# Performance work log

Hardware: AMD Instinct MI355X
Metric: run time of the kernel (lower is better)

The kernel has to match this reference:

```python
import jax, jax.numpy as jnp
import numpy as np

B, FR, T, C = 8, 257, 300, 64
CPP, G, K = 16, 8, 3
EPS = 1e-5


def _ln(x, g, b):
    m = jnp.mean(x, axis=-1, keepdims=True)
    v = jnp.mean((x - m) ** 2, axis=-1, keepdims=True)
    return (x - m) * jax.lax.rsqrt(v + EPS) * g + b


def _freq_conv(x, g, b, w, cb, alpha):
    # x: [N, F, C]
    res = x
    y = _ln(x, g, b).transpose(0, 2, 1)  # [N, C, F]
    y = jax.lax.conv_general_dilated(
        y, w, window_strides=(1,), padding=((K // 2, K // 2),),
        feature_group_count=G, dimension_numbers=("NCH", "OIH", "NCH"))
    y = y + cb[None, :, None]
    y = y.transpose(0, 2, 1)  # [N, F, C]
    return res + jnp.where(y >= 0, y, alpha * y)


def _full_band(x, g, b, rw, rb, fW, fB, ew, eb):
    # x: [N, F, C]
    res = x
    y = _ln(x, g, b)
    hp = jax.nn.silu(jnp.einsum("nfc,pc->nfp", y, rw) + rb)  # [N, F, Cpp]
    hp = hp.transpose(0, 2, 1)  # [N, Cpp, F]
    # batched per-channel Linear(F, F): out[n,c,g] = sum_f hp[n,c,f] * fW[c,g,f] + fB[c,g]
    hp = jnp.einsum("ncf,cgf->ncg", hp, fW) + fB[None]
    hp = hp.transpose(0, 2, 1)  # [N, F, Cpp]
    out = jax.nn.silu(jnp.einsum("nfp,cp->nfc", hp, ew) + eb)
    return res + out


def setup_inputs() -> dict:
    key = jax.random.key(0)
    ks = jax.random.split(key, 20)
    s = 0.05
    d = {
        "h": jax.random.normal(ks[0], (B, FR, T, C), jnp.float32),
        "fc1_g": jnp.ones((C,), jnp.float32),
        "fc1_b": jnp.zeros((C,), jnp.float32),
        "fc1_w": jax.random.normal(ks[1], (C, C // G, K), jnp.float32) * s,
        "fc1_cb": jax.random.normal(ks[2], (C,), jnp.float32) * s,
        "fc1_a": jnp.asarray(0.25, jnp.float32),
        "fbl_g": jnp.ones((C,), jnp.float32),
        "fbl_b": jnp.zeros((C,), jnp.float32),
        "red_w": jax.random.normal(ks[3], (CPP, C), jnp.float32) * s,
        "red_b": jax.random.normal(ks[4], (CPP,), jnp.float32) * s,
        "fW": jax.random.normal(ks[5], (CPP, FR, FR), jnp.float32) * s,
        "fB": jax.random.normal(ks[6], (CPP, FR), jnp.float32) * s,
        "exp_w": jax.random.normal(ks[7], (C, CPP), jnp.float32) * s,
        "exp_b": jax.random.normal(ks[8], (C,), jnp.float32) * s,
        "fc2_g": jnp.ones((C,), jnp.float32),
        "fc2_b": jnp.zeros((C,), jnp.float32),
        "fc2_w": jax.random.normal(ks[9], (C, C // G, K), jnp.float32) * s,
        "fc2_cb": jax.random.normal(ks[10], (C,), jnp.float32) * s,
        "fc2_a": jnp.asarray(0.25, jnp.float32),
    }
    return d


def reference(h, fc1_g, fc1_b, fc1_w, fc1_cb, fc1_a,
              fbl_g, fbl_b, red_w, red_b, fW, fB, exp_w, exp_b,
              fc2_g, fc2_b, fc2_w, fc2_cb, fc2_a):
    b, fr, t, c = h.shape
    x = h.transpose(0, 2, 1, 3).reshape(b * t, fr, c)  # [B*T, F, C]
    x = _freq_conv(x, fc1_g, fc1_b, fc1_w, fc1_cb, fc1_a)
    x = _full_band(x, fbl_g, fbl_b, red_w, red_b, fW, fB, exp_w, exp_b)
    x = _freq_conv(x, fc2_g, fc2_b, fc2_w, fc2_cb, fc2_a)
    return x.reshape(b, t, fr, c).transpose(0, 2, 1, 3)
```

## Files before the change

kernel.cpp:

```cpp
#include <hip/hip_runtime.h>
#include <math.h>

#define BDIM 8
#define FR   257
#define TT   300
#define CC   64
#define NN   (BDIM*TT)
#define CPPC 16
#define GG   8
#define CPG  8
#define KW   3
#define EPSV 1e-5f

#define FT    36
#define NTIL  8
#define ROWS  38
#define FSTR  65
#define NIT   10

#define X1_ELEMS ((size_t)NN*FR*CC)
#define HP_ELEMS ((size_t)CPPC*NN*FR)

template<int CTRL>
__device__ __forceinline__ float dpp_term(float v) {
    return __int_as_float(
        __builtin_amdgcn_update_dpp(0, __float_as_int(v), CTRL, 0xf, 0xf, true));
}
template<int PAT>
__device__ __forceinline__ float swz_term(float v) {
    return __int_as_float(__builtin_amdgcn_ds_swizzle(__float_as_int(v), PAT));
}

__device__ __forceinline__ float wave_sum64(float v) {
    v += dpp_term<0x111>(v);
    v += dpp_term<0x112>(v);
    v += dpp_term<0x114>(v);
    v += dpp_term<0x118>(v);
    v += dpp_term<0x142>(v);
    v += dpp_term<0x143>(v);
    return __int_as_float(__builtin_amdgcn_readlane(__float_as_int(v), 63));
}

__device__ __forceinline__ void ln_stats_dpp(float v, float& m, float& r) {
    float s  = wave_sum64(v);
    float ss = wave_sum64(v*v);
    m = s * (1.0f/64.0f);
    float var = ss * (1.0f/64.0f) - m*m;
    r = rsqrtf(var + EPSV);
}

__device__ __forceinline__ float conv_row(float y0, float y1, float y2,
                                          const float wq[8][KW]) {
    float q[8];
    #pragma unroll
    for (int d = 0; d < 8; ++d)
        q[d] = y0*wq[d][0] + y1*wq[d][1] + y2*wq[d][2];
    float acc = q[0];
    acc += dpp_term<0xB1>(q[1]);
    acc += dpp_term<0x4E>(q[2]);
    acc += dpp_term<0x1B>(q[3]);
    acc += swz_term<0x101F>(q[4]);
    acc += swz_term<0x141F>(q[5]);
    acc += swz_term<0x181F>(q[6]);
    acc += dpp_term<0x141>(q[7]);
    return acc;
}

__global__ __launch_bounds__(256, 8)
void k_fc1(const float* __restrict__ h,
           const float* __restrict__ g1, const float* __restrict__ b1,
           const float* __restrict__ w1, const float* __restrict__ cb1,
           const float* __restrict__ a1,
           const float* __restrict__ g2, const float* __restrict__ b2,
           const float* __restrict__ redw, const float* __restrict__ redb,
           float* __restrict__ x1, float* __restrict__ hpT)
{
    __shared__ float ys[ROWS*FSTR];
    __shared__ float xs[FT*FSTR];

    const int n  = blockIdx.x;
    const int f0 = blockIdx.y * FT;
    const int nf = min(FT, FR - f0);
    const int b = n / TT, t = n - b*TT;
    const int tid = threadIdx.x;
    const int lane = tid & 63, wid = tid >> 6;

    const float alpha = a1[0];
    const float gA = g1[lane], bA = b1[lane];
    const float gB = g2[lane], bB = b2[lane];
    const float cbv = cb1[lane];

    const size_t hb0 = ((size_t)b*FR*TT + t)*CC;
    #pragma unroll
    for (int it = 0; it < NIT; ++it) {
        int lr = wid + it*4;
        if (lr >= ROWS) continue;
        int f = f0 - 1 + lr;
        if (f >= 0 && f < FR) {
            float v = h[hb0 + (size_t)f*TT*CC + lane];
            if (lr >= 1 && lr <= nf) xs[(lr-1)*FSTR + lane] = v;
            float m, r; ln_stats_dpp(v, m, r);
            ys[lr*FSTR + lane] = (v - m) * r * gA + bA;
        } else {
            ys[lr*FSTR + lane] = 0.0f;
        }
    }
    __syncthreads();

    const int l8 = lane & 7;
    const int gbase = lane & 56;
    float wq[8][KW];
    #pragma unroll
    for (int d = 0; d < 8; ++d) {
        const float* wp = w1 + (size_t)(gbase | (l8 ^ d))*(CPG*KW) + l8*KW;
        #pragma unroll
        for (int k = 0; k < KW; ++k) wq[d][k] = wp[k];
    }

    #pragma unroll
    for (int it = 0; it < NIT; ++it) {
        int lr = wid + it*4;
        if (lr < 1 || lr > nf) continue;
        float y0 = ys[(lr-1)*FSTR + lane];
        float y1 = ys[ lr   *FSTR + lane];
        float y2 = ys[(lr+1)*FSTR + lane];
        float acc = conv_row(y0, y1, y2, wq) + cbv;
        float pr = acc >= 0.0f ? acc : alpha*acc;
        float xv = xs[(lr-1)*FSTR + lane] + pr;
        xs[(lr-1)*FSTR + lane] = xv;
        int f = f0 + lr - 1;
        x1[(size_t)n*FR*CC + (size_t)f*CC + lane] = xv;
    }
    __syncthreads();

    #pragma unroll
    for (int it = 0; it < NIT; ++it) {
        int lr = wid + it*4;
        if (lr < 1 || lr > nf) continue;
        float v = xs[(lr-1)*FSTR + lane];
        float m, r; ln_stats_dpp(v, m, r);
        ys[lr*FSTR + lane] = (v - m) * r * gB + bB;
    }
    __syncthreads();

    {
        const int L = lane;
        const int lr = (L < nf) ? (L + 1) : 1;
        const int p0 = wid * 4;
        const float* wp0 = redw + (size_t)(p0+0)*CC;
        const float* wp1 = redw + (size_t)(p0+1)*CC;
        const float* wp2 = redw + (size_t)(p0+2)*CC;
        const float* wp3 = redw + (size_t)(p0+3)*CC;
        float a0 = redb[p0+0], a1v = redb[p0+1], a2 = redb[p0+2], a3 = redb[p0+3];
        #pragma unroll 16
        for (int c = 0; c < CC; ++c) {
            float yv = ys[lr*FSTR + c];
            a0  += yv * wp0[c];
            a1v += yv * wp1[c];
            a2  += yv * wp2[c];
            a3  += yv * wp3[c];
        }
        if (L < nf) {
            int f = f0 + L;
            float s0 = a0  / (1.0f + expf(-a0));
            float s1 = a1v / (1.0f + expf(-a1v));
            float s2 = a2  / (1.0f + expf(-a2));
            float s3 = a3  / (1.0f + expf(-a3));
            size_t base = (size_t)n*FR + f;
            hpT[(size_t)(p0+0)*(NN*FR) + base] = s0;
            hpT[(size_t)(p0+1)*(NN*FR) + base] = s1;
            hpT[(size_t)(p0+2)*(NN*FR) + base] = s2;
            hpT[(size_t)(p0+3)*(NN*FR) + base] = s3;
        }
    }
}

#define GBM 128
#define GBN 64
#define GBK 16
#define GLDA 132
#define GLDB 68

__global__ __launch_bounds__(128, 2)
void k_fgemm(const float* __restrict__ hpT, const float* __restrict__ fW,
             const float* __restrict__ fB, float* __restrict__ hp2T)
{
    __shared__ __align__(16) float As[GBK*GLDA];
    __shared__ __align__(16) float Bs[GBK*GLDB];
    const int c  = blockIdx.z;
    const int m0 = blockIdx.x * GBM;
    const int f0 = blockIdx.y * GBN;
    const int tid = threadIdx.x;
    const int tx = tid & 7;
    const int ty = tid >> 3;

    const float* Ab = hpT + (size_t)c*(NN*FR);
    const float* Bb = fW  + (size_t)c*(FR*FR);

    float acc[8][8];
    #pragma unroll
    for (int i = 0; i < 8; ++i)
        #pragma unroll
        for (int j = 0; j < 8; ++j) acc[i][j] = 0.0f;

    for (int k0 = 0; k0 < FR; k0 += GBK) {
        #pragma unroll
        for (int l = 0; l < 4; ++l) {
            int e = tid + l*128;
            int m = e >> 2, kq = e & 3;
            int gm = m0 + m, gk = k0 + kq*4;
            float4 v = make_float4(0.f,0.f,0.f,0.f);
            if (gm < NN) {
                if (gk + 3 < FR) {
                    v = *reinterpret_cast<const float4*>(&Ab[(size_t)gm*FR + gk]);
                } else {
                    float tv[4] = {0.f,0.f,0.f,0.f};
                    #pragma unroll
                    for (int j = 0; j < 4; ++j) if (gk+j < FR) tv[j] = Ab[(size_t)gm*FR + gk + j];
                    v = make_float4(tv[0],tv[1],tv[2],tv[3]);
                }
            }
            As[(kq*4+0)*GLDA + m] = v.x;
            As[(kq*4+1)*GLDA + m] = v.y;
            As[(kq*4+2)*GLDA + m] = v.z;
            As[(kq*4+3)*GLDA + m] = v.w;
        }
        #pragma unroll
        for (int l = 0; l < 2; ++l) {
            int e = tid + l*128;
            int j = e >> 2, kq = e & 3;
            int gf = f0 + j, gk = k0 + kq*4;
            float4 v = make_float4(0.f,0.f,0.f,0.f);
            if (gf < FR) {
                if (gk + 3 < FR) {
                    v = *reinterpret_cast<const float4*>(&Bb[(size_t)gf*FR + gk]);
                } else {
                    float tv[4] = {0.f,0.f,0.f,0.f};
                    #pragma unroll
                    for (int jj = 0; jj < 4; ++jj) if (gk+jj < FR) tv[jj] = Bb[(size_t)gf*FR + gk + jj];
                    v = make_float4(tv[0],tv[1],tv[2],tv[3]);
                }
            }
            Bs[(kq*4+0)*GLDB + j] = v.x;
            Bs[(kq*4+1)*GLDB + j] = v.y;
            Bs[(kq*4+2)*GLDB + j] = v.z;
            Bs[(kq*4+3)*GLDB + j] = v.w;
        }
        __syncthreads();

        #pragma unroll
        for (int k = 0; k < GBK; ++k) {
            const float4 a0 = *reinterpret_cast<const float4*>(&As[k*GLDA + ty*8]);
            const float4 a1 = *reinterpret_cast<const float4*>(&As[k*GLDA + ty*8 + 4]);
            const float4 b0 = *reinterpret_cast<const float4*>(&Bs[k*GLDB + tx*8]);
            const float4 b1 = *reinterpret_cast<const float4*>(&Bs[k*GLDB + tx*8 + 4]);
            const float av[8] = {a0.x,a0.y,a0.z,a0.w,a1.x,a1.y,a1.z,a1.w};
            const float bv[8] = {b0.x,b0.y,b0.z,b0.w,b1.x,b1.y,b1.z,b1.w};
            #pragma unroll
            for (int i = 0; i < 8; ++i)
                #pragma unroll
                for (int j = 0; j < 8; ++j)
                    acc[i][j] += av[i]*bv[j];
        }
        __syncthreads();
    }

    #pragma unroll
    for (int i = 0; i < 8; ++i) {
        int m = m0 + ty*8 + i;
        if (m >= NN) continue;
        #pragma unroll
        for (int j = 0; j < 8; ++j) {
            int fr = f0 + tx*8 + j;
            if (fr < FR)
                hp2T[(size_t)c*(NN*FR) + (size_t)m*FR + fr] = acc[i][j] + fB[c*FR + fr];
        }
    }
}

__global__ __launch_bounds__(256, 8)
void k_fc2(const float* __restrict__ x1, const float* __restrict__ hp2T,
           const float* __restrict__ expw, const float* __restrict__ expb,
           const float* __restrict__ g3, const float* __restrict__ b3,
           const float* __restrict__ w2, const float* __restrict__ cb2,
           const float* __restrict__ a2,
           float* __restrict__ out)
{
    __shared__ float ys[ROWS*FSTR];
    __shared__ float xs[FT*FSTR];

    const int n  = blockIdx.x;
    const int f0 = blockIdx.y * FT;
    const int nf = min(FT, FR - f0);
    const int b = n / TT, t = n - b*TT;
    const int tid = threadIdx.x;
    const int lane = tid & 63, wid = tid >> 6;

    const float ebv = expb[lane];
    const float gC = g3[lane], bC = b3[lane];
    const float alpha = a2[0];
    const float cbv = cb2[lane];

    float ew[CPPC];
    #pragma unroll
    for (int p = 0; p < CPPC; ++p) ew[p] = expw[lane*CPPC + p];

    #pragma unroll
    for (int it = 0; it < NIT; ++it) {
        int lr = wid + it*4;
        if (lr >= ROWS) continue;
        int f = f0 - 1 + lr;
        if (f >= 0 && f < FR) {
            size_t base = (size_t)n*FR + f;
            float z = ebv;
            #pragma unroll
            for (int p = 0; p < CPPC; ++p)
                z += hp2T[(size_t)p*(NN*FR) + base] * ew[p];
            float sg = z / (1.0f + expf(-z));
            float v = x1[(size_t)n*FR*CC + (size_t)f*CC + lane] + sg;
            if (lr >= 1 && lr <= nf) xs[(lr-1)*FSTR + lane] = v;
            float m, r; ln_stats_dpp(v, m, r);
            ys[lr*FSTR + lane] = (v - m) * r * gC + bC;
        } else {
            ys[lr*FSTR + lane] = 0.0f;
        }
    }
    __syncthreads();

    const int l8 = lane & 7;
    const int gbase = lane & 56;
    float wq[8][KW];
    #pragma unroll
    for (int d = 0; d < 8; ++d) {
        const float* wp = w2 + (size_t)(gbase | (l8 ^ d))*(CPG*KW) + l8*KW;
        #pragma unroll
        for (int k = 0; k < KW; ++k) wq[d][k] = wp[k];
    }

    const size_t ob0 = ((size_t)b*FR*TT + t)*CC;
    #pragma unroll
    for (int it = 0; it < NIT; ++it) {
        int lr = wid + it*4;
        if (lr < 1 || lr > nf) continue;
        float y0 = ys[(lr-1)*FSTR + lane];
        float y1 = ys[ lr   *FSTR + lane];
        float y2 = ys[(lr+1)*FSTR + lane];
        float acc = conv_row(y0, y1, y2, wq) + cbv;
        float pr = acc >= 0.0f ? acc : alpha*acc;
        int f = f0 + lr - 1;
        out[ob0 + (size_t)f*TT*CC + lane] = xs[(lr-1)*FSTR + lane] + pr;
    }
}

extern "C" void kernel_launch(void* const* d_in, const int* in_sizes, int n_in,
                              void* d_out, int out_size, void* d_ws, size_t ws_size,
                              hipStream_t stream) {
    const float* h      = (const float*)d_in[0];
    const float* fc1_g  = (const float*)d_in[1];
    const float* fc1_b  = (const float*)d_in[2];
    const float* fc1_w  = (const float*)d_in[3];
    const float* fc1_cb = (const float*)d_in[4];
    const float* fc1_a  = (const float*)d_in[5];
    const float* fbl_g  = (const float*)d_in[6];
    const float* fbl_b  = (const float*)d_in[7];
    const float* red_w  = (const float*)d_in[8];
    const float* red_b  = (const float*)d_in[9];
    const float* fW     = (const float*)d_in[10];
    const float* fB     = (const float*)d_in[11];
    const float* exp_w  = (const float*)d_in[12];
    const float* exp_b  = (const float*)d_in[13];
    const float* fc2_g  = (const float*)d_in[14];
    const float* fc2_b  = (const float*)d_in[15];
    const float* fc2_w  = (const float*)d_in[16];
    const float* fc2_cb = (const float*)d_in[17];
    const float* fc2_a  = (const float*)d_in[18];

    float* ws   = (float*)d_ws;
    float* x1   = ws;
    float* hpT  = x1 + X1_ELEMS;
    float* hp2T = hpT + HP_ELEMS;

    dim3 g1(NN, NTIL);
    k_fc1<<<g1, 256, 0, stream>>>(h, fc1_g, fc1_b, fc1_w, fc1_cb, fc1_a,
                                  fbl_g, fbl_b, red_w, red_b, x1, hpT);

    dim3 g2((NN + GBM - 1)/GBM, (FR + GBN - 1)/GBN, CPPC);
    k_fgemm<<<g2, 128, 0, stream>>>(hpT, fW, fB, hp2T);

    dim3 g3(NN, NTIL);
    k_fc2<<<g3, 256, 0, stream>>>(x1, hp2T, exp_w, exp_b,
                                  fc2_g, fc2_b, fc2_w, fc2_cb, fc2_a,
                                  (float*)d_out);
}
```

Baseline: 990.4 us.

## Enlarge frequency tiles and process two rows per wave with float2 LayerNorm

Grows the per-block frequency tile in the two conv kernels from 36 to 64 rows, which shrinks the fraction of halo rows that are reloaded and normalised twice. Each wave now handles two rows at once, one per 32-lane half, using float2 global loads and a half-wave DPP/swizzle reduction for the LayerNorm statistics. The load and normalisation loops are restructured to match, and launch bounds are relaxed from 8 to 2 blocks per CU. In exchange each block needs more LDS and the register budget grows, which may lower occupancy, and the tail tile at the end of the frequency axis is partly empty.

```diff
diff --git a/kernel.cpp b/kernel.cpp
--- a/kernel.cpp
+++ b/kernel.cpp
@@ -12,11 +12,10 @@
 #define KW   3
 #define EPSV 1e-5f
 
-#define FT    36
-#define NTIL  8
-#define ROWS  38
+#define FT    64
+#define NTIL  5
+#define ROWS  66
 #define FSTR  65
-#define NIT   10
 
 #define X1_ELEMS ((size_t)NN*FR*CC)
 #define HP_ELEMS ((size_t)CPPC*NN*FR)
@@ -31,19 +30,16 @@
     return __int_as_float(__builtin_amdgcn_ds_swizzle(__float_as_int(v), PAT));
 }
 
-__device__ __forceinline__ float wave_sum64(float v) {
-    v += dpp_term<0x111>(v);
-    v += dpp_term<0x112>(v);
-    v += dpp_term<0x114>(v);
-    v += dpp_term<0x118>(v);
-    v += dpp_term<0x142>(v);
-    v += dpp_term<0x143>(v);
-    return __int_as_float(__builtin_amdgcn_readlane(__float_as_int(v), 63));
-}
-
-__device__ __forceinline__ void ln_stats_dpp(float v, float& m, float& r) {
-    float s  = wave_sum64(v);
-    float ss = wave_sum64(v*v);
+__device__ __forceinline__ void ln_stats_pair(float2 v, float& m, float& r) {
+    float s  = v.x + v.y;
+    float ss = v.x*v.x + v.y*v.y;
+    s += dpp_term<0x111>(s);  ss += dpp_term<0x111>(ss);
+    s += dpp_term<0x112>(s);  ss += dpp_term<0x112>(ss);
+    s += dpp_term<0x114>(s);  ss += dpp_term<0x114>(ss);
+    s += dpp_term<0x118>(s);  ss += dpp_term<0x118>(ss);
+    s += dpp_term<0x142>(s);  ss += dpp_term<0x142>(ss);
+    s  = swz_term<0x03E0>(s);
+    ss = swz_term<0x03E0>(ss);
     m = s * (1.0f/64.0f);
     float var = ss * (1.0f/64.0f) - m*m;
     r = rsqrtf(var + EPSV);
@@ -66,7 +62,14 @@
     return acc;
 }
 
-__global__ __launch_bounds__(256, 8)
+__device__ __forceinline__ void lds_wr2(float* p, int idx, float2 v) {
+    p[idx] = v.x; p[idx+1] = v.y;
+}
+__device__ __forceinline__ float2 lds_rd2(const float* p, int idx) {
+    return make_float2(p[idx], p[idx+1]);
+}
+
+__global__ __launch_bounds__(256, 2)
 void k_fc1(const float* __restrict__ h,
            const float* __restrict__ g1, const float* __restrict__ b1,
            const float* __restrict__ w1, const float* __restrict__ cb1,
@@ -84,25 +87,28 @@
     const int b = n / TT, t = n - b*TT;
     const int tid = threadIdx.x;
     const int lane = tid & 63, wid = tid >> 6;
-
-    const float alpha = a1[0];
-    const float gA = g1[lane], bA = b1[lane];
-    const float gB = g2[lane], bB = b2[lane];
-    const float cbv = cb1[lane];
+    const int hl = lane & 31, half = lane >> 5;
+    const int ch = hl << 1;
+
+    const float2 gA2 = *reinterpret_cast<const float2*>(&g1[ch]);
+    const float2 bA2 = *reinterpret_cast<const float2*>(&b1[ch]);
 
     const size_t hb0 = ((size_t)b*FR*TT + t)*CC;
     #pragma unroll
-    for (int it = 0; it < NIT; ++it) {
-        int lr = wid + it*4;
-        if (lr >= ROWS) continue;
+    for (int it = 0; it < 9; ++it) {
+        int rp = wid + it*4;
+        if (rp >= 33) continue;
+        int lr = 2*rp + half;
         int f = f0 - 1 + lr;
         if (f >= 0 && f < FR) {
-            float v = h[hb0 + (size_t)f*TT*CC + lane];
-            if (lr >= 1 && lr <= nf) xs[(lr-1)*FSTR + lane] = v;
-            float m, r; ln_stats_dpp(v, m, r);
-            ys[lr*FSTR + lane] = (v - m) * r * gA + bA;
+            float2 v = *reinterpret_cast<const float2*>(&h[hb0 + (size_t)f*TT*CC + ch]);
+            if (lr >= 1 && lr <= nf) lds_wr2(xs, (lr-1)*FSTR + ch, v);
+            float m, r; ln_stats_pair(v, m, r);
+            float2 o = make_float2((v.x - m)*r*gA2.x + bA2.x,
+                                   (v.y - m)*r*gA2.y + bA2.y);
+            lds_wr2(ys, lr*FSTR + ch, o);
         } else {
-            ys[lr*FSTR + lane] = 0.0f;
+            lds_wr2(ys, lr*FSTR + ch, make_float2(0.f, 0.f));
         }
     }
     __syncthreads();
@@ -116,9 +122,11 @@
         #pragma unroll
         for (int k = 0; k < KW; ++k) wq[d][k] = wp[k];
     }
-
-    #pragma unroll
-    for (int it = 0; it < NIT; ++it) {
+    const float alpha = a1[0];
+    const float cbv = cb1[lane];
+
+    #pragma unroll
+    for (int it = 0; it < 17; ++it) {
         int lr = wid + it*4;
         if (lr < 1 || lr > nf) continue;
         float y0 = ys[(lr-1)*FSTR + lane];
@@ -133,13 +141,18 @@
     }
     __syncthreads();
 
-    #pragma unroll
-    for (int it = 0; it < NIT; ++it) {
-        int lr = wid + it*4;
-        if (lr < 1 || lr > nf) continue;
-        float v = xs[(lr-1)*FSTR + lane];
-        float m, r; ln_stats_dpp(v, m, r);
-        ys[lr*FSTR + lane] = (v - m) * r * gB + bB;
+    const float2 gB2 = *reinterpret_cast<const float2*>(&g2[ch]);
+    const float2 bB2 = *reinterpret_cast<const float2*>(&b2[ch]);
+    #pragma unroll
+    for (int it = 0; it < 8; ++it) {
+        int rp = wid + it*4;
+        int ir = 2*rp + half;
+        if (ir >= nf) continue;
+        float2 v = lds_rd2(xs, ir*FSTR + ch);
+        float m, r; ln_stats_pair(v, m, r);
+        float2 o = make_float2((v.x - m)*r*gB2.x + bB2.x,
+                               (v.y - m)*r*gB2.y + bB2.y);
+        lds_wr2(ys, (ir+1)*FSTR + ch, o);
     }
     __syncthreads();
 
@@ -278,7 +291,7 @@
     }
 }
 
-__global__ __launch_bounds__(256, 8)
+__global__ __launch_bounds__(256, 2)
 void k_fc2(const float* __restrict__ x1, const float* __restrict__ hp2T,
            const float* __restrict__ expw, const float* __restrict__ expb,
            const float* __restrict__ g3, const float* __restrict__ b3,
@@ -295,34 +308,44 @@
     const int b = n / TT, t = n - b*TT;
     const int tid = threadIdx.x;
     const int lane = tid & 63, wid = tid >> 6;
-
-    const float ebv = expb[lane];
-    const float gC = g3[lane], bC = b3[lane];
-    const float alpha = a2[0];
-    const float cbv = cb2[lane];
-
-    float ew[CPPC];
-    #pragma unroll
-    for (int p = 0; p < CPPC; ++p) ew[p] = expw[lane*CPPC + p];
-
-    #pragma unroll
-    for (int it = 0; it < NIT; ++it) {
-        int lr = wid + it*4;
-        if (lr >= ROWS) continue;
+    const int hl = lane & 31, half = lane >> 5;
+    const int ch = hl << 1;
+
+    const float2 gC2 = *reinterpret_cast<const float2*>(&g3[ch]);
+    const float2 bC2 = *reinterpret_cast<const float2*>(&b3[ch]);
+    const float2 eb2 = *reinterpret_cast<const float2*>(&expb[ch]);
+
+    float2 ew2[CPPC];
+    #pragma unroll
+    for (int p = 0; p < CPPC; ++p)
+        ew2[p] = make_float2(expw[ch*CPPC + p], expw[(ch+1)*CPPC + p]);
+
+    #pragma unroll
+    for (int it = 0; it < 9; ++it) {
+        int rp = wid + it*4;
+        if (rp >= 33) continue;
+        int lr = 2*rp + half;
         int f = f0 - 1 + lr;
         if (f >= 0 && f < FR) {
             size_t base = (size_t)n*FR + f;
-            float z = ebv;
+            float2 z = eb2;
             #pragma unroll
-            for (int p = 0; p < CPPC; ++p)
-                z += hp2T[(size_t)p*(NN*FR) + base] * ew[p];
-            float sg = z / (1.0f + expf(-z));
-            float v = x1[(size_t)n*FR*CC + (size_t)f*CC + lane] + sg;
-            if (lr >= 1 && lr <= nf) xs[(lr-1)*FSTR + lane] = v;
-            float m, r; ln_stats_dpp(v, m, r);
-            ys[lr*FSTR + lane] = (v - m) * r * gC + bC;
+            for (int p = 0; p < CPPC; ++p) {
+                float hp = hp2T[(size_t)p*(NN*FR) + base];
+                z.x += hp * ew2[p].x;
+                z.y += hp * ew2[p].y;
+            }
+            float2 sg = make_float2(z.x / (1.0f + expf(-z.x)),
+                                    z.y / (1.0f + expf(-z.y)));
+            float2 xv = *reinterpret_cast<const float2*>(&x1[(size_t)n*FR*CC + (size_t)f*CC + ch]);
+            float2 v = make_float2(xv.x + sg.x, xv.y + sg.y);
+            if (lr >= 1 && lr <= nf) lds_wr2(xs, (lr-1)*FSTR + ch, v);
+            float m, r; ln_stats_pair(v, m, r);
+            float2 o = make_float2((v.x - m)*r*gC2.x + bC2.x,
+                                   (v.y - m)*r*gC2.y + bC2.y);
+            lds_wr2(ys, lr*FSTR + ch, o);
         } else {
-            ys[lr*FSTR + lane] = 0.0f;
+            lds_wr2(ys, lr*FSTR + ch, make_float2(0.f, 0.f));
         }
     }
     __syncthreads();
@@ -336,10 +359,12 @@
         #pragma unroll
         for (int k = 0; k < KW; ++k) wq[d][k] = wp[k];
     }
+    const float alpha = a2[0];
+    const float cbv = cb2[lane];
 
     const size_t ob0 = ((size_t)b*FR*TT + t)*CC;
     #pragma unroll
-    for (int it = 0; it < NIT; ++it) {
+    for (int it = 0; it < 17; ++it) {
         int lr = wid + it*4;
         if (lr < 1 || lr > nf) continue;
         float y0 = ys[(lr-1)*FSTR + lane];
```

New measurement: 883.5 us. -10.8%, faster.
